# Performance work log

Hardware: AMD Instinct MI355X
Metric: run time of the kernel (lower is better)

## Reference

```python
import jax, jax.numpy as jnp
import numpy as np

EMBED = 1024
HEADS = 16
HEAD_DIM = EMBED // HEADS


def setup_inputs() -> dict:
    key = jax.random.key(0)
    ks = jax.random.split(key, 5)
    s = 1.0 / np.sqrt(EMBED)
    return {
        "x": jax.random.normal(ks[0], (4, 2048, EMBED), dtype=jnp.float32),
        "W_qkv": jax.random.uniform(ks[1], (EMBED, 3 * EMBED), jnp.float32, -s, s),
        "b_qkv": jax.random.uniform(ks[2], (3 * EMBED,), jnp.float32, -s, s),
        "W_out": jax.random.uniform(ks[3], (EMBED, EMBED), jnp.float32, -s, s),
        "b_out": jax.random.uniform(ks[4], (EMBED,), jnp.float32, -s, s),
    }


def reference(x, W_qkv, b_qkv, W_out, b_out):
    B, S, E = x.shape
    qkv = x @ W_qkv + b_qkv  # [B,S,3E]
    q, k, v = jnp.split(qkv, 3, axis=-1)
    # [B,S,E] -> [B,H,S,D]
    def split_heads(t):
        return t.reshape(B, S, HEADS, HEAD_DIM).transpose(0, 2, 1, 3)
    q, k, v = split_heads(q), split_heads(k), split_heads(v)
    scale = 1.0 / jnp.sqrt(jnp.asarray(HEAD_DIM, dtype=x.dtype))
    scores = jnp.einsum("bhqd,bhkd->bhqk", q, k) * scale
    attn = jax.nn.softmax(scores, axis=-1)
    out = jnp.einsum("bhqk,bhkd->bhqd", attn, v)
    out = out.transpose(0, 2, 1, 3).reshape(B, S, E)
    return out @ W_out + b_out
```

## Files before the change

### kernel.cpp

```cpp
#include <hip/hip_runtime.h>
#include <hip/hip_bf16.h>

typedef __bf16 bf16;
typedef __bf16 bf16x8 __attribute__((ext_vector_type(8)));
typedef float f32x4 __attribute__((ext_vector_type(4)));
typedef float f32x16 __attribute__((ext_vector_type(16)));

#define EMB 1024
#define SEQ 2048
#define NH 16
#define HD 64
#define MTOK 8192

__global__ __launch_bounds__(256) void cast_f32_bf16(const float* __restrict__ in,
                                                     bf16* __restrict__ out, int n8) {
    int i = blockIdx.x * blockDim.x + threadIdx.x;
    if (i < n8) {
        const float4* p = (const float4*)in + 2 * (size_t)i;
        float4 a = p[0], b = p[1];
        bf16x8 v;
        v[0] = (bf16)a.x; v[1] = (bf16)a.y; v[2] = (bf16)a.z; v[3] = (bf16)a.w;
        v[4] = (bf16)b.x; v[5] = (bf16)b.y; v[6] = (bf16)b.z; v[7] = (bf16)b.w;
        *(bf16x8*)(out + 8 * (size_t)i) = v;
    }
}

__global__ __launch_bounds__(256) void transpose_cast(const float* __restrict__ W,
                                                      bf16* __restrict__ Wt, int K, int N) {
    __shared__ float tile[32][33];
    int n0 = blockIdx.x * 32, k0 = blockIdx.y * 32;
    int tx = threadIdx.x & 31, ty = threadIdx.x >> 5;
    #pragma unroll
    for (int i = 0; i < 32; i += 8)
        tile[ty + i][tx] = W[(size_t)(k0 + ty + i) * N + n0 + tx];
    __syncthreads();
    #pragma unroll
    for (int i = 0; i < 32; i += 8)
        Wt[(size_t)(n0 + ty + i) * K + k0 + tx] = (bf16)tile[tx][ty + i];
}

#define BM 128
#define BN 128
#define BK 64
#define LDK 72

#define QSCALE 0.1803368801111f

__global__ __launch_bounds__(256) void gemm_qkv(const bf16* __restrict__ A,
                                                const bf16* __restrict__ Bt,
                                                const float* __restrict__ bias,
                                                bf16* __restrict__ qws, bf16* __restrict__ kws,
                                                bf16* __restrict__ vt) {
    __shared__ bf16 sA[BM][LDK];
    __shared__ bf16 sB[BN][LDK];
    const int K = 1024;
    int m0 = blockIdx.x * BM, n0 = blockIdx.y * BN;
    int t = threadIdx.x, lane = t & 63, w = t >> 6;
    int wr = w >> 1, wc = w & 1;
    int l15 = lane & 15, quad = lane >> 4;

    f32x4 acc[4][4];
    #pragma unroll
    for (int i = 0; i < 4; i++)
        #pragma unroll
        for (int j = 0; j < 4; j++) acc[i][j] = (f32x4){0.f, 0.f, 0.f, 0.f};

    int srow = t >> 3, sc8 = (t & 7) * 8;
    for (int kt = 0; kt < K; kt += BK) {
        #pragma unroll
        for (int p = 0; p < 4; p++) {
            int r = srow + p * 32;
            *(uint4*)&sA[r][sc8] = *(const uint4*)(A + (size_t)(m0 + r) * K + kt + sc8);
            *(uint4*)&sB[r][sc8] = *(const uint4*)(Bt + (size_t)(n0 + r) * K + kt + sc8);
        }
        __syncthreads();
        #pragma unroll
        for (int ks = 0; ks < BK; ks += 32) {
            int kk = ks + quad * 8;
            bf16x8 af[4], bfr[4];
            #pragma unroll
            for (int mt = 0; mt < 4; mt++) af[mt] = *(const bf16x8*)&sA[wr * 64 + mt * 16 + l15][kk];
            #pragma unroll
            for (int nt = 0; nt < 4; nt++) bfr[nt] = *(const bf16x8*)&sB[wc * 64 + nt * 16 + l15][kk];
            #pragma unroll
            for (int mt = 0; mt < 4; mt++)
                #pragma unroll
                for (int nt = 0; nt < 4; nt++)
                    acc[mt][nt] = __builtin_amdgcn_mfma_f32_16x16x32_bf16(af[mt], bfr[nt], acc[mt][nt], 0, 0, 0);
        }
        __syncthreads();
    }
    #pragma unroll
    for (int mt = 0; mt < 4; mt++)
        #pragma unroll
        for (int nt = 0; nt < 4; nt++) {
            int col = n0 + wc * 64 + nt * 16 + l15;
            float bv = bias[col];
            int mat = col >> 10;
            int e = col & 1023;
            int h = e >> 6, d = e & 63;
            int row0 = m0 + wr * 64 + mt * 16 + quad * 4;
            int bb = row0 >> 11, s0 = row0 & 2047;
            int bh = bb * NH + h;
            float vv[4];
            #pragma unroll
            for (int r = 0; r < 4; r++) vv[r] = acc[mt][nt][r] + bv;
            if (mat == 0) {
                #pragma unroll
                for (int r = 0; r < 4; r++)
                    qws[((size_t)bh * SEQ + s0 + r) * HD + d] = (bf16)(vv[r] * QSCALE);
            } else if (mat == 1) {
                #pragma unroll
                for (int r = 0; r < 4; r++)
                    kws[((size_t)bh * SEQ + s0 + r) * HD + d] = (bf16)vv[r];
            } else {
                ushort4 pk;
                pk.x = __builtin_bit_cast(unsigned short, (bf16)vv[0]);
                pk.y = __builtin_bit_cast(unsigned short, (bf16)vv[1]);
                pk.z = __builtin_bit_cast(unsigned short, (bf16)vv[2]);
                pk.w = __builtin_bit_cast(unsigned short, (bf16)vv[3]);
                *(ushort4*)((unsigned short*)vt + ((size_t)bh * HD + d) * SEQ + s0) = pk;
            }
        }
}

__device__ __forceinline__ unsigned pk2(float a, float b) {
    unsigned lo = (unsigned)__builtin_bit_cast(unsigned short, (bf16)a);
    unsigned hi = (unsigned)__builtin_bit_cast(unsigned short, (bf16)b);
    return lo | (hi << 16);
}

__global__ __launch_bounds__(256, 4) void attn(const bf16* __restrict__ qws, const bf16* __restrict__ kws,
                                               const bf16* __restrict__ vt, bf16* __restrict__ ao) {
    __shared__ bf16 sK[2][64][72];
    __shared__ bf16 sVt[2][64][72];

    int q0 = blockIdx.x * 128, bh = blockIdx.y;
    int t = threadIdx.x, lane = t & 63, w = t >> 6;
    int l31 = lane & 31, hi = lane >> 5;

    const bf16* qb = qws + (size_t)bh * SEQ * HD;
    const bf16* kb = kws + (size_t)bh * SEQ * HD;
    const bf16* vtb = vt + (size_t)bh * HD * SEQ;

    bf16x8 qf[4];
    #pragma unroll
    for (int ks = 0; ks < 4; ks++)
        qf[ks] = *(const bf16x8*)(qb + (size_t)(q0 + w * 32 + l31) * HD + ks * 16 + hi * 8);

    f32x16 o[2];
    float lsum = 0.f;
    #pragma unroll
    for (int mt = 0; mt < 2; mt++)
        #pragma unroll
        for (int r = 0; r < 16; r++) o[mt][r] = 0.f;

    int krow = t >> 3, kc8 = (t & 7) * 8;
    int vdr = t >> 2, vc16 = (t & 3) * 16;

    {
        uint4 k0 = *(const uint4*)(kb + (size_t)krow * HD + kc8);
        uint4 k1 = *(const uint4*)(kb + (size_t)(krow + 32) * HD + kc8);
        const bf16* src = vtb + (size_t)vdr * SEQ + vc16;
        uint4 v0 = *(const uint4*)src;
        uint4 v1 = *(const uint4*)(src + 8);
        *(uint4*)&sK[0][krow][kc8] = k0;
        *(uint4*)&sK[0][krow + 32][kc8] = k1;
        *(uint4*)&sVt[0][vdr][vc16] = v0;
        *(uint4*)&sVt[0][vdr][vc16 + 8] = v1;
    }

    int cur = 0;
    for (int kv0 = 0; kv0 < SEQ; kv0 += 64) {
        __syncthreads();

        int nxt = kv0 + 64;
        uint4 nk0, nk1, nv0, nv1;
        if (nxt < SEQ) {
            nk0 = *(const uint4*)(kb + (size_t)(nxt + krow) * HD + kc8);
            nk1 = *(const uint4*)(kb + (size_t)(nxt + krow + 32) * HD + kc8);
            const bf16* src = vtb + (size_t)vdr * SEQ + nxt + vc16;
            nv0 = *(const uint4*)src;
            nv1 = *(const uint4*)(src + 8);
        }

        f32x16 sacc[2];
        #pragma unroll
        for (int nt = 0; nt < 2; nt++)
            #pragma unroll
            for (int r = 0; r < 16; r++) sacc[nt][r] = 0.f;
        __builtin_amdgcn_s_setprio(1);
        #pragma unroll
        for (int ks = 0; ks < 4; ks++)
            #pragma unroll
            for (int nt = 0; nt < 2; nt++) {
                bf16x8 kf = *(const bf16x8*)&sK[cur][nt * 32 + l31][ks * 16 + hi * 8];
                sacc[nt] = __builtin_amdgcn_mfma_f32_32x32x16_bf16(kf, qf[ks], sacc[nt], 0, 0, 0);
            }
        __builtin_amdgcn_s_setprio(0);

        bf16x8 pb[4];
        #pragma unroll
        for (int nt = 0; nt < 2; nt++) {
            float e[16];
            #pragma unroll
            for (int r = 0; r < 16; r++) {
                e[r] = __builtin_amdgcn_exp2f(sacc[nt][r]);
                lsum += e[r];
            }
            #pragma unroll
            for (int blk = 0; blk < 2; blk++) {
                int b = blk * 8;
                unsigned a0 = pk2(e[b + 0], e[b + 1]);
                unsigned a1 = pk2(e[b + 2], e[b + 3]);
                unsigned b0 = pk2(e[b + 4], e[b + 5]);
                unsigned b1 = pk2(e[b + 6], e[b + 7]);
                asm("v_permlane32_swap_b32 %0, %1" : "+v"(a0), "+v"(b0));
                asm("v_permlane32_swap_b32 %0, %1" : "+v"(a1), "+v"(b1));
                uint4 f;
                f.x = a0; f.y = a1; f.z = b0; f.w = b1;
                pb[nt * 2 + blk] = __builtin_bit_cast(bf16x8, f);
            }
        }

        __builtin_amdgcn_s_setprio(1);
        #pragma unroll
        for (int s = 0; s < 4; s++)
            #pragma unroll
            for (int mt = 0; mt < 2; mt++) {
                bf16x8 vf = *(const bf16x8*)&sVt[cur][mt * 32 + l31][s * 16 + hi * 8];
                o[mt] = __builtin_amdgcn_mfma_f32_32x32x16_bf16(vf, pb[s], o[mt], 0, 0, 0);
            }
        __builtin_amdgcn_s_setprio(0);

        if (nxt < SEQ) {
            *(uint4*)&sK[cur ^ 1][krow][kc8] = nk0;
            *(uint4*)&sK[cur ^ 1][krow + 32][kc8] = nk1;
            *(uint4*)&sVt[cur ^ 1][vdr][vc16] = nv0;
            *(uint4*)&sVt[cur ^ 1][vdr][vc16 + 8] = nv1;
        }
        cur ^= 1;
    }

    float inv = __builtin_amdgcn_rcpf(lsum + __shfl_xor(lsum, 32));

    int h = bh & 15, bb = bh >> 4;
    int q = q0 + w * 32 + l31;
    #pragma unroll
    for (int mt = 0; mt < 2; mt++)
        #pragma unroll
        for (int g = 0; g < 4; g++) {
            ushort4 pk;
            pk.x = __builtin_bit_cast(unsigned short, (bf16)(o[mt][4 * g + 0] * inv));
            pk.y = __builtin_bit_cast(unsigned short, (bf16)(o[mt][4 * g + 1] * inv));
            pk.z = __builtin_bit_cast(unsigned short, (bf16)(o[mt][4 * g + 2] * inv));
            pk.w = __builtin_bit_cast(unsigned short, (bf16)(o[mt][4 * g + 3] * inv));
            *(ushort4*)((unsigned short*)ao + ((size_t)(bb * SEQ + q)) * EMB + h * HD + mt * 32 + 8 * g + 4 * hi) = pk;
        }
}

__global__ __launch_bounds__(256) void gemm_out(const bf16* __restrict__ A,
                                                const bf16* __restrict__ Bt,
                                                const float* __restrict__ bias,
                                                float* __restrict__ out) {
    __shared__ bf16 sA[BM][LDK];
    __shared__ bf16 sB[BN][LDK];
    const int K = 1024;
    int m0 = blockIdx.x * BM, n0 = blockIdx.y * BN;
    int t = threadIdx.x, lane = t & 63, w = t >> 6;
    int wr = w >> 1, wc = w & 1;
    int l15 = lane & 15, quad = lane >> 4;

    f32x4 acc[4][4];
    #pragma unroll
    for (int i = 0; i < 4; i++)
        #pragma unroll
        for (int j = 0; j < 4; j++) acc[i][j] = (f32x4){0.f, 0.f, 0.f, 0.f};

    int srow = t >> 3, sc8 = (t & 7) * 8;
    for (int kt = 0; kt < K; kt += BK) {
        #pragma unroll
        for (int p = 0; p < 4; p++) {
            int r = srow + p * 32;
            *(uint4*)&sA[r][sc8] = *(const uint4*)(A + (size_t)(m0 + r) * K + kt + sc8);
            *(uint4*)&sB[r][sc8] = *(const uint4*)(Bt + (size_t)(n0 + r) * K + kt + sc8);
        }
        __syncthreads();
        #pragma unroll
        for (int ks = 0; ks < BK; ks += 32) {
            int kk = ks + quad * 8;
            bf16x8 af[4], bfr[4];
            #pragma unroll
            for (int mt = 0; mt < 4; mt++) af[mt] = *(const bf16x8*)&sA[wr * 64 + mt * 16 + l15][kk];
            #pragma unroll
            for (int nt = 0; nt < 4; nt++) bfr[nt] = *(const bf16x8*)&sB[wc * 64 + nt * 16 + l15][kk];
            #pragma unroll
            for (int mt = 0; mt < 4; mt++)
                #pragma unroll
                for (int nt = 0; nt < 4; nt++)
                    acc[mt][nt] = __builtin_amdgcn_mfma_f32_16x16x32_bf16(af[mt], bfr[nt], acc[mt][nt], 0, 0, 0);
        }
        __syncthreads();
    }
    #pragma unroll
    for (int mt = 0; mt < 4; mt++)
        #pragma unroll
        for (int nt = 0; nt < 4; nt++) {
            int col = n0 + wc * 64 + nt * 16 + l15;
            float bv = bias[col];
            #pragma unroll
            for (int r = 0; r < 4; r++) {
                int row = m0 + wr * 64 + mt * 16 + quad * 4 + r;
                out[(size_t)row * EMB + col] = acc[mt][nt][r] + bv;
            }
        }
}

extern "C" void kernel_launch(void* const* d_in, const int* in_sizes, int n_in,
                              void* d_out, int out_size, void* d_ws, size_t ws_size,
                              hipStream_t stream) {
    const float* x     = (const float*)d_in[0];
    const float* W_qkv = (const float*)d_in[1];
    const float* b_qkv = (const float*)d_in[2];
    const float* W_out = (const float*)d_in[3];
    const float* b_out = (const float*)d_in[4];
    float* out = (float*)d_out;

    char* ws = (char*)d_ws;
    bf16* xb    = (bf16*)(ws);
    bf16* wqkvT = (bf16*)(ws + (size_t)(16 << 20));
    bf16* woutT = (bf16*)(ws + (size_t)(22 << 20));
    bf16* qws   = (bf16*)(ws + (size_t)(24 << 20));
    bf16* kws   = (bf16*)(ws + (size_t)(40 << 20));
    bf16* vt    = (bf16*)(ws + (size_t)(56 << 20));
    bf16* aow   = (bf16*)(ws + (size_t)(72 << 20));

    cast_f32_bf16<<<4096, 256, 0, stream>>>(x, xb, MTOK * EMB / 8);
    transpose_cast<<<dim3(3 * EMB / 32, EMB / 32), 256, 0, stream>>>(W_qkv, wqkvT, EMB, 3 * EMB);
    transpose_cast<<<dim3(EMB / 32, EMB / 32), 256, 0, stream>>>(W_out, woutT, EMB, EMB);
    gemm_qkv<<<dim3(MTOK / BM, 3 * EMB / BN), 256, 0, stream>>>(xb, wqkvT, b_qkv, qws, kws, vt);
    attn<<<dim3(SEQ / 128, 64), 256, 0, stream>>>(qws, kws, vt, aow);
    gemm_out<<<dim3(MTOK / BM, EMB / BN), 256, 0, stream>>>(aow, woutT, b_out, out);
}
```

Before: 283.5 us.

## Merge prep kernels into one launch and remap blocks for XCD-aware locality

Folds the x cast and both weight transpose-casts into a single prep kernel, saving two launches. It also remaps linear block IDs in the two GEMMs and the attention kernel so that blocks landing on the same XCD (round-robin by id mod 8) share A rows or the same head. The goal is better L2 reuse per XCD. The cost is more index arithmetic, and the mapping relies on the dispatcher assigning blocks round-robin across 8 XCDs.

```diff
diff --git a/kernel.cpp b/kernel.cpp
--- a/kernel.cpp
+++ b/kernel.cpp
@@ -12,23 +12,33 @@
 #define HD 64
 #define MTOK 8192
 
-__global__ __launch_bounds__(256) void cast_f32_bf16(const float* __restrict__ in,
-                                                     bf16* __restrict__ out, int n8) {
-    int i = blockIdx.x * blockDim.x + threadIdx.x;
-    if (i < n8) {
-        const float4* p = (const float4*)in + 2 * (size_t)i;
+__global__ __launch_bounds__(256) void prep(const float* __restrict__ x, bf16* __restrict__ xb,
+                                            const float* __restrict__ Wq, bf16* __restrict__ WqT,
+                                            const float* __restrict__ Wo, bf16* __restrict__ WoT) {
+    __shared__ float tile[32][33];
+    int bid = blockIdx.x;
+    if (bid < 4096) {
+        int i = bid * 256 + threadIdx.x;
+        const float4* p = (const float4*)x + 2 * (size_t)i;
         float4 a = p[0], b = p[1];
         bf16x8 v;
         v[0] = (bf16)a.x; v[1] = (bf16)a.y; v[2] = (bf16)a.z; v[3] = (bf16)a.w;
         v[4] = (bf16)b.x; v[5] = (bf16)b.y; v[6] = (bf16)b.z; v[7] = (bf16)b.w;
-        *(bf16x8*)(out + 8 * (size_t)i) = v;
-    }
-}
-
-__global__ __launch_bounds__(256) void transpose_cast(const float* __restrict__ W,
-                                                      bf16* __restrict__ Wt, int K, int N) {
-    __shared__ float tile[32][33];
-    int n0 = blockIdx.x * 32, k0 = blockIdx.y * 32;
+        *(bf16x8*)(xb + 8 * (size_t)i) = v;
+        return;
+    }
+    const float* W;
+    bf16* Wt;
+    int K = EMB, N, n0, k0;
+    if (bid < 4096 + 3072) {
+        int i = bid - 4096;
+        W = Wq; Wt = WqT; N = 3 * EMB;
+        n0 = (i % 96) * 32; k0 = (i / 96) * 32;
+    } else {
+        int i = bid - 7168;
+        W = Wo; Wt = WoT; N = EMB;
+        n0 = (i & 31) * 32; k0 = (i >> 5) * 32;
+    }
     int tx = threadIdx.x & 31, ty = threadIdx.x >> 5;
     #pragma unroll
     for (int i = 0; i < 32; i += 8)
@@ -54,7 +64,10 @@
     __shared__ bf16 sA[BM][LDK];
     __shared__ bf16 sB[BN][LDK];
     const int K = 1024;
-    int m0 = blockIdx.x * BM, n0 = blockIdx.y * BN;
+    int lin = blockIdx.x + 64 * blockIdx.y;
+    int a8 = lin & 7, tt = lin >> 3;
+    int mx = (a8 << 3) + (tt & 7), ny = tt >> 3;
+    int m0 = mx * BM, n0 = ny * BN;
     int t = threadIdx.x, lane = t & 63, w = t >> 6;
     int wr = w >> 1, wc = w & 1;
     int l15 = lane & 15, quad = lane >> 4;
@@ -135,7 +148,10 @@
     __shared__ bf16 sK[2][64][72];
     __shared__ bf16 sVt[2][64][72];
 
-    int q0 = blockIdx.x * 128, bh = blockIdx.y;
+    int lin = blockIdx.x + (SEQ / 128) * blockIdx.y;
+    int a8 = lin & 7, tt = lin >> 3;
+    int bh = (a8 << 3) + (tt >> 4);
+    int q0 = (tt & 15) * 128;
     int t = threadIdx.x, lane = t & 63, w = t >> 6;
     int l31 = lane & 31, hi = lane >> 5;
 
@@ -266,7 +282,10 @@
     __shared__ bf16 sA[BM][LDK];
     __shared__ bf16 sB[BN][LDK];
     const int K = 1024;
-    int m0 = blockIdx.x * BM, n0 = blockIdx.y * BN;
+    int lin = blockIdx.x + 64 * blockIdx.y;
+    int a8 = lin & 7, tt = lin >> 3;
+    int mx = (a8 << 3) + (tt & 7), ny = tt >> 3;
+    int m0 = mx * BM, n0 = ny * BN;
     int t = threadIdx.x, lane = t & 63, w = t >> 6;
     int wr = w >> 1, wc = w & 1;
     int l15 = lane & 15, quad = lane >> 4;
@@ -335,9 +354,7 @@
     bf16* vt    = (bf16*)(ws + (size_t)(56 << 20));
     bf16* aow   = (bf16*)(ws + (size_t)(72 << 20));
 
-    cast_f32_bf16<<<4096, 256, 0, stream>>>(x, xb, MTOK * EMB / 8);
-    transpose_cast<<<dim3(3 * EMB / 32, EMB / 32), 256, 0, stream>>>(W_qkv, wqkvT, EMB, 3 * EMB);
-    transpose_cast<<<dim3(EMB / 32, EMB / 32), 256, 0, stream>>>(W_out, woutT, EMB, EMB);
+    prep<<<8192, 256, 0, stream>>>(x, xb, W_qkv, wqkvT, W_out, woutT);
     gemm_qkv<<<dim3(MTOK / BM, 3 * EMB / BN), 256, 0, stream>>>(xb, wqkvT, b_qkv, qws, kws, vt);
     attn<<<dim3(SEQ / 128, 64), 256, 0, stream>>>(qws, kws, vt, aow);
     gemm_out<<<dim3(MTOK / BM, EMB / BN), 256, 0, stream>>>(aow, woutT, b_out, out);
```

Result: faster. 267.5 us (-5.7%).
